# Performance work log

Measured on AMD Instinct MI355X. Metric: run time of the kernel, lower is better.

## Reference

```python
import jax, jax.numpy as jnp
import numpy as np

B, L, S, LA, NA, E, D, H, NHID = 16, 256, 100, 48, 32, 64, 768, 12, 1024
W_IDX = S + 2
EPS = 1e-12


def setup_inputs() -> dict:
    rng = np.random.default_rng(0)
    key = jax.random.key(0)
    ks = jax.random.split(key, 8)
    idxs = np.zeros((B, W_IDX), dtype=np.int64)
    bert_lens = np.zeros((B,), dtype=np.int64)
    is_trig = np.zeros((B, S), dtype=np.float32)
    ent_map = np.zeros((B, S, E), dtype=np.float32)
    argw_mask = np.zeros((B, LA, 1), dtype=np.float32)
    for b in range(B):
        sb = int(rng.integers(60, S + 1))          # n first-subword tokens
        ab = int(rng.integers(8, LA + 1))          # n arg-role subwords
        sent_idx = np.sort(rng.choice(np.arange(1, 2 * sb + 1), size=sb, replace=False))
        sls = 2 * sb + 1                           # second-to-last [SEP] position
        last = sls + ab + 1                        # last [SEP] position
        idxs[b, :sb] = sent_idx
        idxs[b, sb] = sls
        idxs[b, sb + 1] = last
        bert_lens[b] = last + 1
        t0 = int(rng.integers(0, sb - 1))
        is_trig[b, t0:t0 + 2] = 1.0
        eb = int(rng.integers(16, E + 1))
        for e in range(eb):
            ent_map[b, int(rng.integers(0, sb)), e] = 1.0
        argw_mask[b, :ab, 0] = 1.0
    arg_w = np.asarray(jax.random.uniform(ks[0], (B, LA, NA), dtype=jnp.float32)) * argw_mask
    return {
        'all_embeddings': jax.random.normal(ks[1], (B, L, D), dtype=jnp.float32),
        'is_triggers': jnp.asarray(is_trig),
        'arg_weight_matrices': jnp.asarray(arg_w, dtype=jnp.float32),
        'entity_mapping': jnp.asarray(ent_map),
        'att0': jax.random.uniform(ks[2], (B, H, L, L), dtype=jnp.float32),
        'att1': jax.random.uniform(ks[3], (B, H, L, L), dtype=jnp.float32),
        'att2': jax.random.uniform(ks[4], (B, H, L, L), dtype=jnp.float32),
        'W_ta': jax.random.normal(ks[5], (3 * D, D), dtype=jnp.float32) * 0.02,
        'b_ta': jnp.zeros((D,), dtype=jnp.float32),
        'W1': jax.random.normal(ks[6], (6 * D, NHID), dtype=jnp.float32) * 0.02,
        'b1': jnp.zeros((NHID,), dtype=jnp.float32),
        'W2': jax.random.normal(ks[7], (NHID, 1), dtype=jnp.float32) * 0.02,
        'b2': jnp.zeros((1,), dtype=jnp.float32),
        'idxs_to_collect': jnp.asarray(idxs),
        'bert_sentence_lengths': jnp.asarray(bert_lens),
    }


def _l1_normalize(x, axis):
    # F.normalize(x, p=1, dim=axis)
    return x / jnp.clip(jnp.sum(jnp.abs(x), axis=axis, keepdims=True), EPS)


def reference(all_embeddings, is_triggers, arg_weight_matrices, entity_mapping,
              att0, att1, att2, W_ta, b_ta, W1, b1, W2, b2,
              idxs_to_collect, bert_sentence_lengths):
    idxs = idxs_to_collect
    valid = idxs > 0                                   # [B,W]
    n_valid = jnp.sum(valid, axis=1)                   # [B]
    j = jnp.arange(S)
    sent_valid = (j[None, :] < (n_valid - 2)[:, None]).astype(all_embeddings.dtype)  # [B,S]
    sent_idx = idxs[:, :S]
    # first-subword gather, zero-padded (get_fist_subword_embeddings)
    sent_emb = jnp.take_along_axis(all_embeddings, sent_idx[:, :, None], axis=1) * sent_valid[:, :, None]
    # arg-role segment: (second_last_sep+1) .. (bert_len-2), zero-padded to LA
    sls = jnp.take_along_axis(idxs, (n_valid - 2)[:, None], axis=1)[:, 0]   # [B]
    arg_pos = sls[:, None] + 1 + jnp.arange(LA)[None, :]                    # [B,LA]
    arg_valid = (arg_pos < (bert_sentence_lengths - 1)[:, None]).astype(all_embeddings.dtype)
    arg_emb0 = jnp.take_along_axis(all_embeddings, jnp.clip(arg_pos, 0, L - 1)[:, :, None], axis=1) * arg_valid[:, :, None]
    # entity aggregation + trigger mean pooling
    entity = jnp.einsum('bsd,bse->bed', sent_emb, entity_mapping)           # [B,E,D]
    trig = jnp.sum(sent_emb * is_triggers[:, :, None], axis=1) / jnp.sum(is_triggers, axis=1)[:, None]
    arg = jnp.einsum('bld,bla->bad', arg_emb0, arg_weight_matrices)         # [B,NA,D]
    # trigger-aware entity fusion
    trig_e = jnp.broadcast_to(trig[:, None, :], entity.shape)
    nonempty = (jnp.sum(jnp.abs(entity), axis=-1) > 0).astype(entity.dtype)
    ent_cat = jnp.concatenate([entity, trig_e, entity * trig_e], axis=-1)   # [B,E,3D]
    entity = (ent_cat @ W_ta + b_ta) * nonempty[:, :, None]
    # bidirectional token<->arg attention (L1-normalized)
    score = jnp.einsum('bed,bad->bea', entity, arg) / np.sqrt(D)            # [B,E,NA]
    t2a = _l1_normalize(score, 2)[..., None]
    a2t = _l1_normalize(score, 1)[..., None]
    token_argAwared = jnp.sum(arg[:, None] * t2a, axis=2)                   # [B,E,D]
    arg_tokenAwared = jnp.sum(entity[:, :, None] * a2t, axis=1)             # [B,NA,D]
    # select_hidden_att: head-mean, gather collected rows/cols, row-renormalize
    def sel_att(att):
        m = jnp.mean(att, axis=1)                                           # [B,L,L]
        r = jnp.take_along_axis(m, sent_idx[:, :, None], axis=1)            # [B,S,L]
        c = jnp.take_along_axis(r, sent_idx[:, None, :], axis=2)            # [B,S,S]
        c = c * sent_valid[:, :, None] * sent_valid[:, None, :]
        return c / jnp.clip(jnp.sum(c, axis=-1, keepdims=True), EPS)
    t2t = (sel_att(att0) + sel_att(att1) + sel_att(att2)) / 3.0             # [B,S,S]
    a_h2h_tok = t2t @ sent_emb                                              # [B,S,D]
    A_h2h = jnp.einsum('bse,bsd->bed', entity_mapping, a_h2h_tok)           # [B,E,D]
    H_ = jnp.einsum('bse,bsd->bed', entity_mapping, sent_emb)               # [B,E,D]
    a2a = jax.nn.softmax(arg @ jnp.swapaxes(arg, -1, -2), axis=-1)
    A_u2u = a2a @ arg                                                       # [B,NA,D]
    shp = (B, E, NA, D)
    latent = jnp.concatenate([
        jnp.broadcast_to(H_[:, :, None], shp),
        jnp.broadcast_to(arg[:, None], shp),
        jnp.broadcast_to(token_argAwared[:, :, None], shp),
        jnp.broadcast_to(A_h2h[:, :, None], shp),
        jnp.broadcast_to(arg_tokenAwared[:, None], shp),
        jnp.broadcast_to(A_u2u[:, None], shp),
    ], axis=-1)                                                             # [B,E,NA,6D]
    h = jax.nn.gelu(latent @ W1 + b1, approximate=False)
    out = (h @ W2 + b2)[..., 0]                                             # [B,E,NA]
    return out
```

## Files before the change

kernel.cpp:

```cpp
#include <hip/hip_runtime.h>
#include <math.h>

#define B_ 16
#define L_ 256
#define S_ 100
#define LA_ 48
#define NA_ 32
#define E_ 64
#define D_ 768
#define H_ 12
#define NHID_ 1024
#define WIDX_ 102
#define EPSF 1e-12f

typedef __attribute__((ext_vector_type(8))) short s16x8;
typedef __attribute__((ext_vector_type(4))) float f32x4;

__device__ __forceinline__ void split_bf16(float x, unsigned short& h, unsigned short& l) {
  unsigned u = __float_as_uint(x);
  unsigned hr = u + 0x7FFFu + ((u >> 16) & 1u);
  h = (unsigned short)(hr >> 16);
  float r = x - __uint_as_float(hr & 0xFFFF0000u);
  unsigned u2 = __float_as_uint(r);
  unsigned lr = u2 + 0x7FFFu + ((u2 >> 16) & 1u);
  l = (unsigned short)(lr >> 16);
}

__global__ void k_meta(const int* __restrict__ idxs, const int* __restrict__ blen,
                       int* __restrict__ meta) {
  int b = blockIdx.x, t = threadIdx.x;
  __shared__ int cnt;
  if (t == 0) cnt = 0;
  __syncthreads();
  if (t < WIDX_ && idxs[b * WIDX_ + t] > 0) atomicAdd(&cnt, 1);
  __syncthreads();
  if (t == 0) {
    int sb = cnt - 2;
    meta[b * 4 + 0] = sb;
    meta[b * 4 + 1] = idxs[b * WIDX_ + sb];
    meta[b * 4 + 2] = blen[b] - 1;
  }
}

__global__ void k_gather(const float* __restrict__ emb, const int* __restrict__ idxs,
                         const int* __restrict__ meta, float* __restrict__ sent_emb,
                         float* __restrict__ arg_emb) {
  int b = blockIdx.y, y = blockIdx.x, t = threadIdx.x;
  int sb = meta[b * 4 + 0], sls = meta[b * 4 + 1], last = meta[b * 4 + 2];
  if (y < S_) {
    int s = y;
    float* dst = sent_emb + ((size_t)b * S_ + s) * D_;
    if (s < sb) {
      const float* src = emb + ((size_t)b * L_ + idxs[b * WIDX_ + s]) * D_;
      for (int d = t; d < D_; d += 256) dst[d] = src[d];
    } else {
      for (int d = t; d < D_; d += 256) dst[d] = 0.f;
    }
  } else {
    int l = y - S_;
    int pos = sls + 1 + l;
    float* dst = arg_emb + ((size_t)b * LA_ + l) * D_;
    if (pos < last) {
      int p = pos > (L_ - 1) ? (L_ - 1) : pos;
      const float* src = emb + ((size_t)b * L_ + p) * D_;
      for (int d = t; d < D_; d += 256) dst[d] = src[d];
    } else {
      for (int d = t; d < D_; d += 256) dst[d] = 0.f;
    }
  }
}

__global__ void k_trig(const float* __restrict__ sent_emb, const float* __restrict__ is_trig,
                       float* __restrict__ trig) {
  int b = blockIdx.y;
  int d = blockIdx.x * 256 + threadIdx.x;
  float acc = 0.f, den = 0.f;
  for (int s = 0; s < S_; s++) {
    float w = is_trig[b * S_ + s];
    den += w;
    if (w != 0.f) acc += w * sent_emb[((size_t)b * S_ + s) * D_ + d];
  }
  trig[b * D_ + d] = acc / den;
}

__global__ __launch_bounds__(256) void k_entity0(const float* __restrict__ sent_emb,
                                                 const float* __restrict__ ent_map,
                                                 const float* __restrict__ trig,
                                                 unsigned short* __restrict__ e0h,
                                                 unsigned short* __restrict__ e0l,
                                                 unsigned short* __restrict__ e0th,
                                                 unsigned short* __restrict__ e0tl,
                                                 float* __restrict__ ne) {
  int b = blockIdx.y, e = blockIdx.x, t = threadIdx.x;
  float a0 = 0.f, a1 = 0.f, a2 = 0.f;
  for (int s = 0; s < S_; s++) {
    float w = ent_map[((size_t)b * S_ + s) * E_ + e];
    if (w != 0.f) {
      const float* r = sent_emb + ((size_t)b * S_ + s) * D_;
      a0 += w * r[t]; a1 += w * r[t + 256]; a2 += w * r[t + 512];
    }
  }
  size_t o = ((size_t)b * E_ + e) * D_;
  const float* tr = trig + b * D_;
  unsigned short h, lo;
  split_bf16(a0, h, lo); e0h[o + t] = h; e0l[o + t] = lo;
  split_bf16(a1, h, lo); e0h[o + t + 256] = h; e0l[o + t + 256] = lo;
  split_bf16(a2, h, lo); e0h[o + t + 512] = h; e0l[o + t + 512] = lo;
  split_bf16(a0 * tr[t], h, lo); e0th[o + t] = h; e0tl[o + t] = lo;
  split_bf16(a1 * tr[t + 256], h, lo); e0th[o + t + 256] = h; e0tl[o + t + 256] = lo;
  split_bf16(a2 * tr[t + 512], h, lo); e0th[o + t + 512] = h; e0tl[o + t + 512] = lo;
  __shared__ float red[256];
  red[t] = fabsf(a0) + fabsf(a1) + fabsf(a2);
  __syncthreads();
  for (int s2 = 128; s2 > 0; s2 >>= 1) {
    if (t < s2) red[t] += red[t + s2];
    __syncthreads();
  }
  if (t == 0) ne[b * E_ + e] = (red[0] > 0.f) ? 1.f : 0.f;
}

__global__ __launch_bounds__(256) void k_wsum(const float* __restrict__ Wm, int wstride, int sy,
                                              int sx, const float* __restrict__ Vm,
                                              float* __restrict__ Om,
                                              unsigned short* __restrict__ oh,
                                              unsigned short* __restrict__ ol, int Y) {
  int b = blockIdx.y, x = blockIdx.x, t = threadIdx.x;
  float a0 = 0.f, a1 = 0.f, a2 = 0.f;
  const float* wb = Wm + (size_t)b * wstride + (size_t)x * sx;
  const float* vb = Vm + (size_t)b * Y * D_;
  for (int y = 0; y < Y; y++) {
    float w = wb[(size_t)y * sy];
    if (w != 0.f) {
      const float* r = vb + (size_t)y * D_;
      a0 += w * r[t]; a1 += w * r[t + 256]; a2 += w * r[t + 512];
    }
  }
  size_t oidx = ((size_t)b * gridDim.x + x) * D_;
  if (Om) {
    Om[oidx + t] = a0; Om[oidx + t + 256] = a1; Om[oidx + t + 512] = a2;
  }
  if (oh) {
    unsigned short h, lo;
    split_bf16(a0, h, lo); oh[oidx + t] = h; ol[oidx + t] = lo;
    split_bf16(a1, h, lo); oh[oidx + t + 256] = h; ol[oidx + t + 256] = lo;
    split_bf16(a2, h, lo); oh[oidx + t + 512] = h; ol[oidx + t + 512] = lo;
  }
}

__global__ void k_tb(const float* __restrict__ trig, const float* __restrict__ W_ta,
                     const float* __restrict__ b_ta, float* __restrict__ tb) {
  int b = blockIdx.y;
  int d = blockIdx.x * 256 + threadIdx.x;
  float acc0 = b_ta[d], acc1 = 0.f, acc2 = 0.f, acc3 = 0.f;
  float acc4 = 0.f, acc5 = 0.f, acc6 = 0.f, acc7 = 0.f;
  const float* tr = trig + b * D_;
  const float* w = W_ta + (size_t)D_ * D_ + d;
  for (int k = 0; k < D_; k += 8) {
    acc0 += tr[k + 0] * w[(size_t)(k + 0) * D_];
    acc1 += tr[k + 1] * w[(size_t)(k + 1) * D_];
    acc2 += tr[k + 2] * w[(size_t)(k + 2) * D_];
    acc3 += tr[k + 3] * w[(size_t)(k + 3) * D_];
    acc4 += tr[k + 4] * w[(size_t)(k + 4) * D_];
    acc5 += tr[k + 5] * w[(size_t)(k + 5) * D_];
    acc6 += tr[k + 6] * w[(size_t)(k + 6) * D_];
    acc7 += tr[k + 7] * w[(size_t)(k + 7) * D_];
  }
  tb[b * D_ + d] = ((acc0 + acc1) + (acc2 + acc3)) + ((acc4 + acc5) + (acc6 + acc7));
}

__global__ __launch_bounds__(256) void k_cvtT(const float* __restrict__ src, int K, int N,
                                              unsigned short* __restrict__ th,
                                              unsigned short* __restrict__ tl) {
  __shared__ float tile[32][33];
  int k0 = blockIdx.x * 32, n0 = blockIdx.y * 32;
  int tr = threadIdx.x >> 3, c4 = (threadIdx.x & 7) * 4;
  float4 v = *(const float4*)(src + (size_t)(k0 + tr) * N + n0 + c4);
  tile[tr][c4] = v.x; tile[tr][c4 + 1] = v.y; tile[tr][c4 + 2] = v.z; tile[tr][c4 + 3] = v.w;
  __syncthreads();
  unsigned short h[4], l[4];
#pragma unroll
  for (int i = 0; i < 4; ++i) split_bf16(tile[c4 + i][tr], h[i], l[i]);
  size_t oo = (size_t)(n0 + tr) * K + k0 + c4;
  th[oo + 0] = h[0]; th[oo + 1] = h[1]; th[oo + 2] = h[2]; th[oo + 3] = h[3];
  tl[oo + 0] = l[0]; tl[oo + 1] = l[1]; tl[oo + 2] = l[2]; tl[oo + 3] = l[3];
}

__global__ __launch_bounds__(256) void k_mgemm(
    int phase,
    const unsigned short* __restrict__ e0h, const unsigned short* __restrict__ e0l,
    const unsigned short* __restrict__ e0th, const unsigned short* __restrict__ e0tl,
    const unsigned short* __restrict__ Ah2hh, const unsigned short* __restrict__ Ah2hl,
    const unsigned short* __restrict__ argmh, const unsigned short* __restrict__ argml,
    const unsigned short* __restrict__ Au2uh, const unsigned short* __restrict__ Au2ul,
    const unsigned short* __restrict__ WtaTh, const unsigned short* __restrict__ WtaTl,
    const unsigned short* __restrict__ W1Th, const unsigned short* __restrict__ W1Tl,
    float* __restrict__ entn, unsigned short* __restrict__ entnh,
    unsigned short* __restrict__ entnl,
    float* __restrict__ PeA, float* __restrict__ PaA,
    float* __restrict__ P2, float* __restrict__ Q2,
    const float* __restrict__ tb, const float* __restrict__ ne) {
  int z = blockIdx.z;
  const unsigned short *A0h_, *A0l_, *A1h_, *A1l_, *Bh_, *Bl_;
  float* C;
  int koff0, koff1, bstride, mtiles, niter, N, ep = 0;
  if (phase == 0) {
    if (z == 0) {
      A0h_ = e0h; A0l_ = e0l; A1h_ = e0th; A1l_ = e0tl; Bh_ = WtaTh; Bl_ = WtaTl;
      bstride = 2304; koff0 = 0; koff1 = 1536; C = entn; N = 768; mtiles = 16; niter = 48; ep = 1;
    } else if (z == 1) {
      A0h_ = e0h; A0l_ = e0l; A1h_ = Ah2hh; A1l_ = Ah2hl; Bh_ = W1Th; Bl_ = W1Tl;
      bstride = 4608; koff0 = 0; koff1 = 3 * 768; C = PeA; N = 1024; mtiles = 16; niter = 48;
    } else if (z == 2) {
      A0h_ = argmh; A0l_ = argml; A1h_ = Au2uh; A1l_ = Au2ul; Bh_ = W1Th; Bl_ = W1Tl;
      bstride = 4608; koff0 = 768; koff1 = 5 * 768; C = PaA; N = 1024; mtiles = 8; niter = 48;
    } else {
      A0h_ = argmh; A0l_ = argml; A1h_ = argmh; A1l_ = argml; Bh_ = W1Th; Bl_ = W1Tl;
      bstride = 4608; koff0 = 2 * 768; koff1 = 2 * 768; C = P2; N = 1024; mtiles = 8; niter = 24;
    }
  } else {
    A0h_ = entnh; A0l_ = entnl; A1h_ = entnh; A1l_ = entnl; Bh_ = W1Th; Bl_ = W1Tl;
    bstride = 4608; koff0 = 4 * 768; koff1 = 4 * 768; C = Q2; N = 1024; mtiles = 16; niter = 24;
  }
  int bx = blockIdx.x, by = blockIdx.y;
  if (by >= mtiles || bx * 64 >= N) return;

  __shared__ unsigned short As[2][64][4][8];
  __shared__ unsigned short Bs[2][64][4][8];

  int tid = threadIdx.x;
  int srow = tid >> 2, sg = tid & 3;
  int wc = sg ^ ((srow >> 1) & 3);
  size_t aoff = (size_t)(by * 64 + srow) * 768 + sg * 8;
  size_t brow = (size_t)(bx * 64 + srow) * bstride + sg * 8;
  size_t boff0 = brow + koff0, boff1 = brow + koff1;

  s16x8 rAh = *(const s16x8*)(A0h_ + aoff);
  s16x8 rAl = *(const s16x8*)(A0l_ + aoff);
  s16x8 rBh = *(const s16x8*)(Bh_ + boff0);
  s16x8 rBl = *(const s16x8*)(Bl_ + boff0);

  int lane = tid & 63, wave = tid >> 6;
  int wm = wave >> 1, wn = wave & 1;
  int fg = lane >> 4, fr = lane & 15;
  int ar0 = wm * 32 + fr;
  int bc0 = wn * 32 + fr;
  int ca = fg ^ ((ar0 >> 1) & 3);
  int cb = fg ^ ((bc0 >> 1) & 3);

  f32x4 acc00 = {0.f, 0.f, 0.f, 0.f}, acc01 = {0.f, 0.f, 0.f, 0.f};
  f32x4 acc10 = {0.f, 0.f, 0.f, 0.f}, acc11 = {0.f, 0.f, 0.f, 0.f};

  for (int it = 0; it < niter; ++it) {
    __syncthreads();
    *(s16x8*)&As[0][srow][wc][0] = rAh;
    *(s16x8*)&As[1][srow][wc][0] = rAl;
    *(s16x8*)&Bs[0][srow][wc][0] = rBh;
    *(s16x8*)&Bs[1][srow][wc][0] = rBl;
    __syncthreads();
    if (it + 1 < niter) {
      int l = it + 1;
      int p = (l >= 24) ? 1 : 0;
      size_t ka = (size_t)(l - (p ? 24 : 0)) * 32;
      rAh = *(const s16x8*)((p ? A1h_ : A0h_) + aoff + ka);
      rAl = *(const s16x8*)((p ? A1l_ : A0l_) + aoff + ka);
      size_t bo = (p ? boff1 : boff0) + ka;
      rBh = *(const s16x8*)(Bh_ + bo);
      rBl = *(const s16x8*)(Bl_ + bo);
    }
    s16x8 ah0 = *(const s16x8*)&As[0][ar0][ca][0];
    s16x8 ah1 = *(const s16x8*)&As[0][ar0 + 16][ca][0];
    s16x8 al0 = *(const s16x8*)&As[1][ar0][ca][0];
    s16x8 al1 = *(const s16x8*)&As[1][ar0 + 16][ca][0];
    s16x8 bh0 = *(const s16x8*)&Bs[0][bc0][cb][0];
    s16x8 bh1 = *(const s16x8*)&Bs[0][bc0 + 16][cb][0];
    s16x8 bl0 = *(const s16x8*)&Bs[1][bc0][cb][0];
    s16x8 bl1 = *(const s16x8*)&Bs[1][bc0 + 16][cb][0];
    acc00 = __builtin_amdgcn_mfma_f32_16x16x32_bf16(ah0, bh0, acc00, 0, 0, 0);
    acc00 = __builtin_amdgcn_mfma_f32_16x16x32_bf16(ah0, bl0, acc00, 0, 0, 0);
    acc00 = __builtin_amdgcn_mfma_f32_16x16x32_bf16(al0, bh0, acc00, 0, 0, 0);
    acc01 = __builtin_amdgcn_mfma_f32_16x16x32_bf16(ah0, bh1, acc01, 0, 0, 0);
    acc01 = __builtin_amdgcn_mfma_f32_16x16x32_bf16(ah0, bl1, acc01, 0, 0, 0);
    acc01 = __builtin_amdgcn_mfma_f32_16x16x32_bf16(al0, bh1, acc01, 0, 0, 0);
    acc10 = __builtin_amdgcn_mfma_f32_16x16x32_bf16(ah1, bh0, acc10, 0, 0, 0);
    acc10 = __builtin_amdgcn_mfma_f32_16x16x32_bf16(ah1, bl0, acc10, 0, 0, 0);
    acc10 = __builtin_amdgcn_mfma_f32_16x16x32_bf16(al1, bh0, acc10, 0, 0, 0);
    acc11 = __builtin_amdgcn_mfma_f32_16x16x32_bf16(ah1, bh1, acc11, 0, 0, 0);
    acc11 = __builtin_amdgcn_mfma_f32_16x16x32_bf16(ah1, bl1, acc11, 0, 0, 0);
    acc11 = __builtin_amdgcn_mfma_f32_16x16x32_bf16(al1, bh1, acc11, 0, 0, 0);
  }

  f32x4 accs[2][2] = {{acc00, acc01}, {acc10, acc11}};
  int colb = bx * 64 + wn * 32 + fr;
  int rowb = by * 64 + wm * 32 + fg * 4;
#pragma unroll
  for (int i = 0; i < 2; ++i) {
#pragma unroll
    for (int j = 0; j < 2; ++j) {
      int col = colb + j * 16;
#pragma unroll
      for (int r = 0; r < 4; ++r) {
        int row = rowb + i * 16 + r;
        float v = accs[i][j][r];
        if (ep == 1) {
          v = (v + tb[(row >> 6) * D_ + col]) * ne[row];
          unsigned short hh, ll;
          split_bf16(v, hh, ll);
          entnh[(size_t)row * D_ + col] = hh;
          entnl[(size_t)row * D_ + col] = ll;
        }
        C[(size_t)row * N + col] = v;
      }
    }
  }
}

__global__ __launch_bounds__(256) void k_score(const float* __restrict__ entn,
                                               const float* __restrict__ argm,
                                               float* __restrict__ score) {
  int b = blockIdx.y, e = blockIdx.x, t = threadIdx.x;
  __shared__ float ent[D_];
  const float* er = entn + ((size_t)b * E_ + e) * D_;
  for (int d = t; d < D_; d += 256) ent[d] = er[d];
  __syncthreads();
  int wave = t >> 6, lane = t & 63;
  const float scale = 0.03608439182435161f;
  for (int a = wave; a < NA_; a += 4) {
    const float* ar = argm + ((size_t)b * NA_ + a) * D_;
    float p = 0.f;
#pragma unroll
    for (int i = 0; i < 12; i++) {
      int d = lane + 64 * i;
      p += ent[d] * ar[d];
    }
    for (int off = 32; off > 0; off >>= 1) p += __shfl_down(p, off);
    if (lane == 0) score[((size_t)b * E_ + e) * NA_ + a] = p * scale;
  }
}

__global__ void k_norm(const float* __restrict__ score, float* __restrict__ t2a,
                       float* __restrict__ a2t) {
  int b = blockIdx.x, t = threadIdx.x;
  __shared__ float s[E_ * NA_];
  __shared__ float rs[E_];
  __shared__ float cs[NA_];
  for (int i = t; i < E_ * NA_; i += 256) s[i] = score[(size_t)b * E_ * NA_ + i];
  __syncthreads();
  if (t < E_) {
    float sum = 0.f;
    for (int a = 0; a < NA_; a++) sum += fabsf(s[t * NA_ + a]);
    rs[t] = fmaxf(sum, EPSF);
  } else if (t >= 64 && t < 96) {
    int a = t - 64;
    float sum = 0.f;
    for (int e = 0; e < E_; e++) sum += fabsf(s[e * NA_ + a]);
    cs[a] = fmaxf(sum, EPSF);
  }
  __syncthreads();
  for (int i = t; i < E_ * NA_; i += 256) {
    int e = i >> 5, a = i & 31;
    float v = s[i];
    t2a[(size_t)b * E_ * NA_ + i] = v / rs[e];
    a2t[(size_t)b * E_ * NA_ + i] = v / cs[a];
  }
}

__global__ __launch_bounds__(256) void k_a2a(const float* __restrict__ argm,
                                             float* __restrict__ a2a) {
  int b = blockIdx.y, a = blockIdx.x, t = threadIdx.x;
  __shared__ float sA[D_];
  __shared__ float lg[NA_];
  const float* ar = argm + ((size_t)b * NA_ + a) * D_;
  for (int d = t; d < D_; d += 256) sA[d] = ar[d];
  __syncthreads();
  int wave = t >> 6, lane = t & 63;
  for (int a2 = wave; a2 < NA_; a2 += 4) {
    const float* br = argm + ((size_t)b * NA_ + a2) * D_;
    float p = 0.f;
#pragma unroll
    for (int i = 0; i < 12; i++) {
      int d = lane + 64 * i;
      p += sA[d] * br[d];
    }
    for (int off = 32; off > 0; off >>= 1) p += __shfl_down(p, off);
    if (lane == 0) lg[a2] = p;
  }
  __syncthreads();
  if (t < 64) {
    float v = (t < NA_) ? lg[t] : -INFINITY;
    float m = v;
    for (int mask = 16; mask > 0; mask >>= 1) m = fmaxf(m, __shfl_xor(m, mask));
    float ex = (t < NA_) ? expf(v - m) : 0.f;
    float sm = ex;
    for (int mask = 16; mask > 0; mask >>= 1) sm += __shfl_xor(sm, mask);
    if (t < NA_) a2a[((size_t)b * NA_ + a) * NA_ + t] = ex / sm;
  }
}

__global__ __launch_bounds__(128) void k_t2t(const float* __restrict__ att0,
                                             const float* __restrict__ att1,
                                             const float* __restrict__ att2,
                                             const int* __restrict__ idxs,
                                             const int* __restrict__ meta,
                                             float* __restrict__ t2t) {
  int b = blockIdx.y, s = blockIdx.x, t = threadIdx.x;
  int sb = meta[b * 4 + 0];
  float* out = t2t + ((size_t)b * S_ + s) * S_;
  if (s >= sb) {
    for (int j = t; j < S_; j += 128) out[j] = 0.f;
    return;
  }
  int Is = idxs[b * WIDX_ + s];
  int It = (t < S_) ? idxs[b * WIDX_ + t] : 0;
  __shared__ float row[256];
  __shared__ float red[128];
  const float* atts[3] = {att0, att1, att2};
  float accout = 0.f;
  for (int q = 0; q < 3; q++) {
    float r0 = 0.f, r1 = 0.f;
    const float* base = atts[q] + (((size_t)b * H_) * L_ + Is) * L_;
    for (int h = 0; h < H_; h++) {
      const float* rp = base + (size_t)h * L_ * L_;
      r0 += rp[t];
      r1 += rp[t + 128];
    }
    row[t] = r0;
    row[t + 128] = r1;
    __syncthreads();
    float v = (t < sb) ? row[It] * (1.f / 12.f) : 0.f;
    red[t] = v;
    __syncthreads();
    for (int s2 = 64; s2 > 0; s2 >>= 1) {
      if (t < s2) red[t] += red[t + s2];
      __syncthreads();
    }
    float rsum = red[0];
    __syncthreads();
    accout += v / fmaxf(rsum, EPSF) * (1.f / 3.f);
  }
  if (t < S_) out[t] = accout;
}

__global__ __launch_bounds__(256) void k_mix(const float* __restrict__ PeA,
                                             const float* __restrict__ PaA,
                                             const float* __restrict__ P2,
                                             const float* __restrict__ Q2,
                                             const float* __restrict__ t2a,
                                             const float* __restrict__ a2t,
                                             const float* __restrict__ b1,
                                             float* __restrict__ ps, float* __restrict__ qs) {
  int b = blockIdx.y, x = blockIdx.x, t = threadIdx.x;
  int n0 = t * 4;
  __shared__ float w[E_];
  if (x < E_) {
    int e = x;
    size_t ro = ((size_t)b * E_ + e) * NHID_ + n0;
    float4 acc = *(const float4*)(PeA + ro);
    float4 bb = *(const float4*)(b1 + n0);
    acc.x += bb.x; acc.y += bb.y; acc.z += bb.z; acc.w += bb.w;
    if (t < NA_) w[t] = t2a[((size_t)b * E_ + e) * NA_ + t];
    __syncthreads();
    const float* pb = P2 + (size_t)b * NA_ * NHID_ + n0;
#pragma unroll 4
    for (int a = 0; a < NA_; a++) {
      float ww = w[a];
      float4 p = *(const float4*)(pb + (size_t)a * NHID_);
      acc.x += ww * p.x; acc.y += ww * p.y; acc.z += ww * p.z; acc.w += ww * p.w;
    }
    *(float4*)(ps + ro) = acc;
  } else {
    int a = x - E_;
    size_t ro = ((size_t)b * NA_ + a) * NHID_ + n0;
    float4 acc = *(const float4*)(PaA + ro);
    for (int i = t; i < E_; i += 256) w[i] = a2t[((size_t)b * E_ + i) * NA_ + a];
    __syncthreads();
    const float* qb = Q2 + (size_t)b * E_ * NHID_ + n0;
#pragma unroll 4
    for (int e = 0; e < E_; e++) {
      float ww = w[e];
      float4 q = *(const float4*)(qb + (size_t)e * NHID_);
      acc.x += ww * q.x; acc.y += ww * q.y; acc.z += ww * q.z; acc.w += ww * q.w;
    }
    *(float4*)(qs + ro) = acc;
  }
}

__global__ __launch_bounds__(256) void k_final(const float* __restrict__ ps,
                                               const float* __restrict__ qs,
                                               const float* __restrict__ W2,
                                               const float* __restrict__ b2,
                                               float* __restrict__ out) {
  int b = blockIdx.y, e = blockIdx.x, t = threadIdx.x;
  int wave = t >> 6, lane = t & 63;
  const float ks = 0.70710678118654752f;
  size_t po = ((size_t)b * E_ + e) * NHID_ + lane * 4;
  float4 p0 = *(const float4*)(ps + po);
  float4 p1 = *(const float4*)(ps + po + 256);
  float4 p2 = *(const float4*)(ps + po + 512);
  float4 p3 = *(const float4*)(ps + po + 768);
  const float* w2p = W2 + lane * 4;
  float4 w0 = *(const float4*)(w2p);
  float4 w1 = *(const float4*)(w2p + 256);
  float4 w2 = *(const float4*)(w2p + 512);
  float4 w3 = *(const float4*)(w2p + 768);
  __shared__ float outs[NA_];
#pragma unroll 2
  for (int a = wave; a < NA_; a += 4) {
    size_t qo = ((size_t)b * NA_ + a) * NHID_ + lane * 4;
    float4 q0 = *(const float4*)(qs + qo);
    float4 q1 = *(const float4*)(qs + qo + 256);
    float4 q2 = *(const float4*)(qs + qo + 512);
    float4 q3 = *(const float4*)(qs + qo + 768);
    float acc = 0.f;
#define GEL4(pp, qq, ww)                                          \
    {                                                             \
      float x0 = pp.x + qq.x, x1 = pp.y + qq.y;                   \
      float x2 = pp.z + qq.z, x3 = pp.w + qq.w;                   \
      float g0 = 0.5f * x0 * (1.f + erff(x0 * ks));               \
      float g1 = 0.5f * x1 * (1.f + erff(x1 * ks));               \
      float g2 = 0.5f * x2 * (1.f + erff(x2 * ks));               \
      float g3 = 0.5f * x3 * (1.f + erff(x3 * ks));               \
      acc += g0 * ww.x + g1 * ww.y + g2 * ww.z + g3 * ww.w;       \
    }
    GEL4(p0, q0, w0)
    GEL4(p1, q1, w1)
    GEL4(p2, q2, w2)
    GEL4(p3, q3, w3)
#undef GEL4
    acc += __shfl_xor(acc, 32);
    acc += __shfl_xor(acc, 16);
    acc += __shfl_xor(acc, 8);
    acc += __shfl_xor(acc, 4);
    acc += __shfl_xor(acc, 2);
    acc += __shfl_xor(acc, 1);
    if (lane == 0) outs[a] = acc;
  }
  __syncthreads();
  if (t < NA_) out[((size_t)b * E_ + e) * NA_ + t] = outs[t] + b2[0];
}

extern "C" void kernel_launch(void* const* d_in, const int* in_sizes, int n_in,
                              void* d_out, int out_size, void* d_ws, size_t ws_size,
                              hipStream_t stream) {
  const float* emb    = (const float*)d_in[0];
  const float* istrig = (const float*)d_in[1];
  const float* argw   = (const float*)d_in[2];
  const float* entmap = (const float*)d_in[3];
  const float* att0   = (const float*)d_in[4];
  const float* att1   = (const float*)d_in[5];
  const float* att2   = (const float*)d_in[6];
  const float* W_ta   = (const float*)d_in[7];
  const float* b_ta   = (const float*)d_in[8];
  const float* W1     = (const float*)d_in[9];
  const float* b1     = (const float*)d_in[10];
  const float* W2     = (const float*)d_in[11];
  const float* b2     = (const float*)d_in[12];
  const int*   idxs   = (const int*)d_in[13];
  const int*   blen   = (const int*)d_in[14];
  float* out = (float*)d_out;

  float* ws = (float*)d_ws;
  size_t o = 0;
  int* meta = (int*)ws; o += 256;
  float* sent_emb = ws + o; o += (size_t)B_ * S_ * D_;
  float* arg_emb  = ws + o; o += (size_t)B_ * LA_ * D_;
  float* trig     = ws + o; o += (size_t)B_ * D_;
  float* argm     = ws + o; o += (size_t)B_ * NA_ * D_;
  float* entn     = ws + o; o += (size_t)B_ * E_ * D_;
  float* tb       = ws + o; o += (size_t)B_ * D_;
  float* ne       = ws + o; o += (size_t)B_ * E_;
  float* score    = ws + o; o += (size_t)B_ * E_ * NA_;
  float* t2a      = ws + o; o += (size_t)B_ * E_ * NA_;
  float* a2t      = ws + o; o += (size_t)B_ * E_ * NA_;
  float* t2t      = ws + o; o += (size_t)B_ * S_ * S_;
  float* ah2h     = ws + o; o += (size_t)B_ * S_ * D_;
  float* a2a      = ws + o; o += (size_t)B_ * NA_ * NA_;
  float* PeA      = ws + o; o += (size_t)B_ * E_ * NHID_;
  float* PaA      = ws + o; o += (size_t)B_ * NA_ * NHID_;
  float* P2       = ws + o; o += (size_t)B_ * NA_ * NHID_;
  float* Q2       = ws + o; o += (size_t)B_ * E_ * NHID_;
  float* ps = sent_emb;
  float* qs = arg_emb;

  o = (o + 3) & ~(size_t)3;
  unsigned short* us = (unsigned short*)(ws + o);
  size_t uo = 0;
  unsigned short* e0h   = us + uo; uo += (size_t)B_ * E_ * D_;
  unsigned short* e0l   = us + uo; uo += (size_t)B_ * E_ * D_;
  unsigned short* e0th  = us + uo; uo += (size_t)B_ * E_ * D_;
  unsigned short* e0tl  = us + uo; uo += (size_t)B_ * E_ * D_;
  unsigned short* Ah2hh = us + uo; uo += (size_t)B_ * E_ * D_;
  unsigned short* Ah2hl = us + uo; uo += (size_t)B_ * E_ * D_;
  unsigned short* argmh = us + uo; uo += (size_t)B_ * NA_ * D_;
  unsigned short* argml = us + uo; uo += (size_t)B_ * NA_ * D_;
  unsigned short* Au2uh = us + uo; uo += (size_t)B_ * NA_ * D_;
  unsigned short* Au2ul = us + uo; uo += (size_t)B_ * NA_ * D_;
  unsigned short* entnh = us + uo; uo += (size_t)B_ * E_ * D_;
  unsigned short* entnl = us + uo; uo += (size_t)B_ * E_ * D_;
  unsigned short* WtaTh = us + uo; uo += (size_t)2304 * 768;
  unsigned short* WtaTl = us + uo; uo += (size_t)2304 * 768;
  unsigned short* W1Th  = us + uo; uo += (size_t)4608 * 1024;
  unsigned short* W1Tl  = us + uo; uo += (size_t)4608 * 1024;

  k_meta<<<B_, 128, 0, stream>>>(idxs, blen, meta);
  k_cvtT<<<dim3(2304 / 32, 768 / 32), 256, 0, stream>>>(W_ta, 2304, 768, WtaTh, WtaTl);
  k_cvtT<<<dim3(4608 / 32, 1024 / 32), 256, 0, stream>>>(W1, 4608, 1024, W1Th, W1Tl);
  k_gather<<<dim3(S_ + LA_, B_), 256, 0, stream>>>(emb, idxs, meta, sent_emb, arg_emb);
  k_trig<<<dim3(3, B_), 256, 0, stream>>>(sent_emb, istrig, trig);
  k_entity0<<<dim3(E_, B_), 256, 0, stream>>>(sent_emb, entmap, trig, e0h, e0l, e0th, e0tl, ne);
  k_wsum<<<dim3(NA_, B_), 256, 0, stream>>>(argw, LA_ * NA_, NA_, 1, arg_emb, argm, argmh,
                                            argml, LA_);
  k_tb<<<dim3(3, B_), 256, 0, stream>>>(trig, W_ta, b_ta, tb);
  k_t2t<<<dim3(S_, B_), 128, 0, stream>>>(att0, att1, att2, idxs, meta, t2t);
  k_wsum<<<dim3(S_, B_), 256, 0, stream>>>(t2t, S_ * S_, 1, S_, sent_emb, ah2h, nullptr,
                                           nullptr, S_);
  k_wsum<<<dim3(E_, B_), 256, 0, stream>>>(entmap, S_ * E_, E_, 1, ah2h, nullptr, Ah2hh,
                                           Ah2hl, S_);
  k_a2a<<<dim3(NA_, B_), 256, 0, stream>>>(argm, a2a);
  k_wsum<<<dim3(NA_, B_), 256, 0, stream>>>(a2a, NA_ * NA_, 1, NA_, argm, nullptr, Au2uh,
                                            Au2ul, NA_);

  k_mgemm<<<dim3(16, 16, 4), 256, 0, stream>>>(0, e0h, e0l, e0th, e0tl, Ah2hh, Ah2hl, argmh,
                                               argml, Au2uh, Au2ul, WtaTh, WtaTl, W1Th, W1Tl,
                                               entn, entnh, entnl, PeA, PaA, P2, Q2, tb, ne);

  k_mgemm<<<dim3(16, 16, 1), 256, 0, stream>>>(1, e0h, e0l, e0th, e0tl, Ah2hh, Ah2hl, argmh,
                                               argml, Au2uh, Au2ul, WtaTh, WtaTl, W1Th, W1Tl,
                                               entn, entnh, entnl, PeA, PaA, P2, Q2, tb, ne);

  k_score<<<dim3(E_, B_), 256, 0, stream>>>(entn, argm, score);
  k_norm<<<B_, 256, 0, stream>>>(score, t2a, a2t);
  k_mix<<<dim3(E_ + NA_, B_), 256, 0, stream>>>(PeA, PaA, P2, Q2, t2a, a2t, b1, ps, qs);

  k_final<<<dim3(E_, B_), 256, 0, stream>>>(ps, qs, W2, b2, out);
}
```

Before: 504.9 us.

## Split-K the batched MFMA GEMMs and double-buffer LDS tiles

Each GEMM job in k_mgemm is split into two K halves run as separate z-slices, which doubles the number of blocks. Each half writes a partial result to its own buffer. The partials are summed later, in a new k_combE kernel for the entity projection and inside k_mix for the W1 partials. The main loop now uses double-buffered LDS with register prefetch two tiles ahead, so it needs one barrier per tile instead of two. The aim is better occupancy on the small 64x64-tile grids and shorter per-block latency, at the cost of extra partial-buffer traffic and one more launch.

```diff
diff --git a/kernel.cpp b/kernel.cpp
--- a/kernel.cpp
+++ b/kernel.cpp
@@ -192,52 +192,55 @@
     const unsigned short* __restrict__ Ah2hh, const unsigned short* __restrict__ Ah2hl,
     const unsigned short* __restrict__ argmh, const unsigned short* __restrict__ argml,
     const unsigned short* __restrict__ Au2uh, const unsigned short* __restrict__ Au2ul,
+    const unsigned short* __restrict__ entnh, const unsigned short* __restrict__ entnl,
     const unsigned short* __restrict__ WtaTh, const unsigned short* __restrict__ WtaTl,
     const unsigned short* __restrict__ W1Th, const unsigned short* __restrict__ W1Tl,
-    float* __restrict__ entn, unsigned short* __restrict__ entnh,
-    unsigned short* __restrict__ entnl,
-    float* __restrict__ PeA, float* __restrict__ PaA,
-    float* __restrict__ P2, float* __restrict__ Q2,
-    const float* __restrict__ tb, const float* __restrict__ ne) {
+    float* __restrict__ Cpe, float* __restrict__ PeAp, float* __restrict__ PaAp,
+    float* __restrict__ P2p, float* __restrict__ Q2p) {
   int z = blockIdx.z;
-  const unsigned short *A0h_, *A0l_, *A1h_, *A1l_, *Bh_, *Bl_;
+  const unsigned short *Ah_, *Al_, *Bh_, *Bl_;
   float* C;
-  int koff0, koff1, bstride, mtiles, niter, N, ep = 0;
+  int bstride, mtiles, niter, N, akoff, bkoff;
+  const size_t HPE = (size_t)B_ * E_ * NHID_;
+  const size_t HPA = (size_t)B_ * NA_ * NHID_;
   if (phase == 0) {
-    if (z == 0) {
-      A0h_ = e0h; A0l_ = e0l; A1h_ = e0th; A1l_ = e0tl; Bh_ = WtaTh; Bl_ = WtaTl;
-      bstride = 2304; koff0 = 0; koff1 = 1536; C = entn; N = 768; mtiles = 16; niter = 48; ep = 1;
-    } else if (z == 1) {
-      A0h_ = e0h; A0l_ = e0l; A1h_ = Ah2hh; A1l_ = Ah2hl; Bh_ = W1Th; Bl_ = W1Tl;
-      bstride = 4608; koff0 = 0; koff1 = 3 * 768; C = PeA; N = 1024; mtiles = 16; niter = 48;
-    } else if (z == 2) {
-      A0h_ = argmh; A0l_ = argml; A1h_ = Au2uh; A1l_ = Au2ul; Bh_ = W1Th; Bl_ = W1Tl;
-      bstride = 4608; koff0 = 768; koff1 = 5 * 768; C = PaA; N = 1024; mtiles = 8; niter = 48;
+    int job = z >> 1, kh = z & 1;
+    if (job == 0) {
+      Ah_ = kh ? e0th : e0h; Al_ = kh ? e0tl : e0l; Bh_ = WtaTh; Bl_ = WtaTl;
+      bstride = 2304; akoff = 0; bkoff = kh ? 1536 : 0;
+      C = Cpe + (size_t)kh * 1024 * 768; N = 768; mtiles = 16; niter = 24;
+    } else if (job == 1) {
+      Ah_ = kh ? Ah2hh : e0h; Al_ = kh ? Ah2hl : e0l; Bh_ = W1Th; Bl_ = W1Tl;
+      bstride = 4608; akoff = 0; bkoff = kh ? 3 * 768 : 0;
+      C = PeAp + kh * HPE; N = 1024; mtiles = 16; niter = 24;
+    } else if (job == 2) {
+      Ah_ = kh ? Au2uh : argmh; Al_ = kh ? Au2ul : argml; Bh_ = W1Th; Bl_ = W1Tl;
+      bstride = 4608; akoff = 0; bkoff = kh ? 5 * 768 : 768;
+      C = PaAp + kh * HPA; N = 1024; mtiles = 8; niter = 24;
     } else {
-      A0h_ = argmh; A0l_ = argml; A1h_ = argmh; A1l_ = argml; Bh_ = W1Th; Bl_ = W1Tl;
-      bstride = 4608; koff0 = 2 * 768; koff1 = 2 * 768; C = P2; N = 1024; mtiles = 8; niter = 24;
+      Ah_ = argmh; Al_ = argml; Bh_ = W1Th; Bl_ = W1Tl;
+      bstride = 4608; akoff = kh * 384; bkoff = 2 * 768 + kh * 384;
+      C = P2p + kh * HPA; N = 1024; mtiles = 8; niter = 12;
     }
   } else {
-    A0h_ = entnh; A0l_ = entnl; A1h_ = entnh; A1l_ = entnl; Bh_ = W1Th; Bl_ = W1Tl;
-    bstride = 4608; koff0 = 4 * 768; koff1 = 4 * 768; C = Q2; N = 1024; mtiles = 16; niter = 24;
+    int kh = z;
+    Ah_ = entnh; Al_ = entnl; Bh_ = W1Th; Bl_ = W1Tl;
+    bstride = 4608; akoff = kh * 384; bkoff = 4 * 768 + kh * 384;
+    C = Q2p + kh * HPE; N = 1024; mtiles = 16; niter = 12;
   }
   int bx = blockIdx.x, by = blockIdx.y;
   if (by >= mtiles || bx * 64 >= N) return;
 
-  __shared__ unsigned short As[2][64][4][8];
-  __shared__ unsigned short Bs[2][64][4][8];
+  __shared__ unsigned short As[2][2][64][4][8];
+  __shared__ unsigned short Bs[2][2][64][4][8];
 
   int tid = threadIdx.x;
   int srow = tid >> 2, sg = tid & 3;
   int wc = sg ^ ((srow >> 1) & 3);
-  size_t aoff = (size_t)(by * 64 + srow) * 768 + sg * 8;
-  size_t brow = (size_t)(bx * 64 + srow) * bstride + sg * 8;
-  size_t boff0 = brow + koff0, boff1 = brow + koff1;
-
-  s16x8 rAh = *(const s16x8*)(A0h_ + aoff);
-  s16x8 rAl = *(const s16x8*)(A0l_ + aoff);
-  s16x8 rBh = *(const s16x8*)(Bh_ + boff0);
-  s16x8 rBl = *(const s16x8*)(Bl_ + boff0);
+  const unsigned short* aPh = Ah_ + (size_t)(by * 64 + srow) * 768 + akoff + sg * 8;
+  const unsigned short* aPl = Al_ + (size_t)(by * 64 + srow) * 768 + akoff + sg * 8;
+  const unsigned short* bPh = Bh_ + (size_t)(bx * 64 + srow) * bstride + bkoff + sg * 8;
+  const unsigned short* bPl = Bl_ + (size_t)(bx * 64 + srow) * bstride + bkoff + sg * 8;
 
   int lane = tid & 63, wave = tid >> 6;
   int wm = wave >> 1, wn = wave & 1;
@@ -250,44 +253,70 @@
   f32x4 acc00 = {0.f, 0.f, 0.f, 0.f}, acc01 = {0.f, 0.f, 0.f, 0.f};
   f32x4 acc10 = {0.f, 0.f, 0.f, 0.f}, acc11 = {0.f, 0.f, 0.f, 0.f};
 
-  for (int it = 0; it < niter; ++it) {
-    __syncthreads();
-    *(s16x8*)&As[0][srow][wc][0] = rAh;
-    *(s16x8*)&As[1][srow][wc][0] = rAl;
-    *(s16x8*)&Bs[0][srow][wc][0] = rBh;
-    *(s16x8*)&Bs[1][srow][wc][0] = rBl;
-    __syncthreads();
+  s16x8 a0h = *(const s16x8*)(aPh + 0), a0l = *(const s16x8*)(aPl + 0);
+  s16x8 b0h = *(const s16x8*)(bPh + 0), b0l = *(const s16x8*)(bPl + 0);
+  s16x8 a1h = *(const s16x8*)(aPh + 32), a1l = *(const s16x8*)(aPl + 32);
+  s16x8 b1h = *(const s16x8*)(bPh + 32), b1l = *(const s16x8*)(bPl + 32);
+
+#define WRITE_LDS(buf, ah, al, bh, bl)              \
+  {                                                 \
+    *(s16x8*)&As[buf][0][srow][wc][0] = ah;         \
+    *(s16x8*)&As[buf][1][srow][wc][0] = al;         \
+    *(s16x8*)&Bs[buf][0][srow][wc][0] = bh;         \
+    *(s16x8*)&Bs[buf][1][srow][wc][0] = bl;         \
+  }
+#define LOAD_SET(ah, al, bh, bl, t_)                \
+  {                                                 \
+    ah = *(const s16x8*)(aPh + (t_) * 32);          \
+    al = *(const s16x8*)(aPl + (t_) * 32);          \
+    bh = *(const s16x8*)(bPh + (t_) * 32);          \
+    bl = *(const s16x8*)(bPl + (t_) * 32);          \
+  }
+#define READ_MFMA(buf)                                                          \
+  {                                                                             \
+    s16x8 xah0 = *(const s16x8*)&As[buf][0][ar0][ca][0];                        \
+    s16x8 xah1 = *(const s16x8*)&As[buf][0][ar0 + 16][ca][0];                   \
+    s16x8 xal0 = *(const s16x8*)&As[buf][1][ar0][ca][0];                        \
+    s16x8 xal1 = *(const s16x8*)&As[buf][1][ar0 + 16][ca][0];                   \
+    s16x8 xbh0 = *(const s16x8*)&Bs[buf][0][bc0][cb][0];                        \
+    s16x8 xbh1 = *(const s16x8*)&Bs[buf][0][bc0 + 16][cb][0];                   \
+    s16x8 xbl0 = *(const s16x8*)&Bs[buf][1][bc0][cb][0];                        \
+    s16x8 xbl1 = *(const s16x8*)&Bs[buf][1][bc0 + 16][cb][0];                   \
+    acc00 = __builtin_amdgcn_mfma_f32_16x16x32_bf16(xah0, xbh0, acc00, 0, 0, 0); \
+    acc00 = __builtin_amdgcn_mfma_f32_16x16x32_bf16(xah0, xbl0, acc00, 0, 0, 0); \
+    acc00 = __builtin_amdgcn_mfma_f32_16x16x32_bf16(xal0, xbh0, acc00, 0, 0, 0); \
+    acc01 = __builtin_amdgcn_mfma_f32_16x16x32_bf16(xah0, xbh1, acc01, 0, 0, 0); \
+    acc01 = __builtin_amdgcn_mfma_f32_16x16x32_bf16(xah0, xbl1, acc01, 0, 0, 0); \
+    acc01 = __builtin_amdgcn_mfma_f32_16x16x32_bf16(xal0, xbh1, acc01, 0, 0, 0); \
+    acc10 = __builtin_amdgcn_mfma_f32_16x16x32_bf16(xah1, xbh0, acc10, 0, 0, 0); \
+    acc10 = __builtin_amdgcn_mfma_f32_16x16x32_bf16(xah1, xbl0, acc10, 0, 0, 0); \
+    acc10 = __builtin_amdgcn_mfma_f32_16x16x32_bf16(xal1, xbh0, acc10, 0, 0, 0); \
+    acc11 = __builtin_amdgcn_mfma_f32_16x16x32_bf16(xah1, xbh1, acc11, 0, 0, 0); \
+    acc11 = __builtin_amdgcn_mfma_f32_16x16x32_bf16(xah1, xbl1, acc11, 0, 0, 0); \
+    acc11 = __builtin_amdgcn_mfma_f32_16x16x32_bf16(xal1, xbh1, acc11, 0, 0, 0); \
+  }
+
+  WRITE_LDS(0, a0h, a0l, b0h, b0l);
+  LOAD_SET(a0h, a0l, b0h, b0l, 2);
+  __syncthreads();
+
+  for (int it = 0; it < niter; it += 2) {
     if (it + 1 < niter) {
-      int l = it + 1;
-      int p = (l >= 24) ? 1 : 0;
-      size_t ka = (size_t)(l - (p ? 24 : 0)) * 32;
-      rAh = *(const s16x8*)((p ? A1h_ : A0h_) + aoff + ka);
-      rAl = *(const s16x8*)((p ? A1l_ : A0l_) + aoff + ka);
-      size_t bo = (p ? boff1 : boff0) + ka;
-      rBh = *(const s16x8*)(Bh_ + bo);
-      rBl = *(const s16x8*)(Bl_ + bo);
-    }
-    s16x8 ah0 = *(const s16x8*)&As[0][ar0][ca][0];
-    s16x8 ah1 = *(const s16x8*)&As[0][ar0 + 16][ca][0];
-    s16x8 al0 = *(const s16x8*)&As[1][ar0][ca][0];
-    s16x8 al1 = *(const s16x8*)&As[1][ar0 + 16][ca][0];
-    s16x8 bh0 = *(const s16x8*)&Bs[0][bc0][cb][0];
-    s16x8 bh1 = *(const s16x8*)&Bs[0][bc0 + 16][cb][0];
-    s16x8 bl0 = *(const s16x8*)&Bs[1][bc0][cb][0];
-    s16x8 bl1 = *(const s16x8*)&Bs[1][bc0 + 16][cb][0];
-    acc00 = __builtin_amdgcn_mfma_f32_16x16x32_bf16(ah0, bh0, acc00, 0, 0, 0);
-    acc00 = __builtin_amdgcn_mfma_f32_16x16x32_bf16(ah0, bl0, acc00, 0, 0, 0);
-    acc00 = __builtin_amdgcn_mfma_f32_16x16x32_bf16(al0, bh0, acc00, 0, 0, 0);
-    acc01 = __builtin_amdgcn_mfma_f32_16x16x32_bf16(ah0, bh1, acc01, 0, 0, 0);
-    acc01 = __builtin_amdgcn_mfma_f32_16x16x32_bf16(ah0, bl1, acc01, 0, 0, 0);
-    acc01 = __builtin_amdgcn_mfma_f32_16x16x32_bf16(al0, bh1, acc01, 0, 0, 0);
-    acc10 = __builtin_amdgcn_mfma_f32_16x16x32_bf16(ah1, bh0, acc10, 0, 0, 0);
-    acc10 = __builtin_amdgcn_mfma_f32_16x16x32_bf16(ah1, bl0, acc10, 0, 0, 0);
-    acc10 = __builtin_amdgcn_mfma_f32_16x16x32_bf16(al1, bh0, acc10, 0, 0, 0);
-    acc11 = __builtin_amdgcn_mfma_f32_16x16x32_bf16(ah1, bh1, acc11, 0, 0, 0);
-    acc11 = __builtin_amdgcn_mfma_f32_16x16x32_bf16(ah1, bl1, acc11, 0, 0, 0);
-    acc11 = __builtin_amdgcn_mfma_f32_16x16x32_bf16(al1, bh1, acc11, 0, 0, 0);
-  }
+      WRITE_LDS(1, a1h, a1l, b1h, b1l);
+      if (it + 3 < niter) LOAD_SET(a1h, a1l, b1h, b1l, it + 3);
+    }
+    READ_MFMA(0);
+    __syncthreads();
+    if (it + 2 < niter) {
+      WRITE_LDS(0, a0h, a0l, b0h, b0l);
+      if (it + 4 < niter) LOAD_SET(a0h, a0l, b0h, b0l, it + 4);
+    }
+    READ_MFMA(1);
+    __syncthreads();
+  }
+#undef WRITE_LDS
+#undef LOAD_SET
+#undef READ_MFMA
 
   f32x4 accs[2][2] = {{acc00, acc01}, {acc10, acc11}};
   int colb = bx * 64 + wn * 32 + fr;
@@ -300,16 +329,35 @@
 #pragma unroll
       for (int r = 0; r < 4; ++r) {
         int row = rowb + i * 16 + r;
-        float v = accs[i][j][r];
-        if (ep == 1) {
-          v = (v + tb[(row >> 6) * D_ + col]) * ne[row];
-          unsigned short hh, ll;
-          split_bf16(v, hh, ll);
-          entnh[(size_t)row * D_ + col] = hh;
-          entnl[(size_t)row * D_ + col] = ll;
-        }
-        C[(size_t)row * N + col] = v;
+        C[(size_t)row * N + col] = accs[i][j][r];
       }
+    }
+  }
+}
+
+__global__ __launch_bounds__(256) void k_combE(const float* __restrict__ Cpe,
+                                               const float* __restrict__ tb,
+                                               const float* __restrict__ ne,
+                                               float* __restrict__ entn,
+                                               unsigned short* __restrict__ entnh,
+                                               unsigned short* __restrict__ entnl) {
+  int t = threadIdx.x;
+  int r0 = blockIdx.x * 4;
+  const size_t HH = (size_t)1024 * 768;
+#pragma unroll
+  for (int i = 0; i < 4; ++i) {
+    int row = r0 + i;
+    int b = row >> 6;
+    float nev = ne[row];
+#pragma unroll
+    for (int j = 0; j < 3; ++j) {
+      int col = t + j * 256;
+      size_t o = (size_t)row * D_ + col;
+      float v = (Cpe[o] + Cpe[HH + o] + tb[(size_t)b * D_ + col]) * nev;
+      entn[o] = v;
+      unsigned short hh, ll;
+      split_bf16(v, hh, ll);
+      entnh[o] = hh; entnl[o] = ll;
     }
   }
 }
@@ -440,45 +488,55 @@
   if (t < S_) out[t] = accout;
 }
 
-__global__ __launch_bounds__(256) void k_mix(const float* __restrict__ PeA,
-                                             const float* __restrict__ PaA,
-                                             const float* __restrict__ P2,
-                                             const float* __restrict__ Q2,
+__global__ __launch_bounds__(256) void k_mix(const float* __restrict__ PeAp,
+                                             const float* __restrict__ PaAp,
+                                             const float* __restrict__ P2p,
+                                             const float* __restrict__ Q2p,
                                              const float* __restrict__ t2a,
                                              const float* __restrict__ a2t,
                                              const float* __restrict__ b1,
                                              float* __restrict__ ps, float* __restrict__ qs) {
   int b = blockIdx.y, x = blockIdx.x, t = threadIdx.x;
   int n0 = t * 4;
+  const size_t HPE = (size_t)B_ * E_ * NHID_;
+  const size_t HPA = (size_t)B_ * NA_ * NHID_;
   __shared__ float w[E_];
   if (x < E_) {
     int e = x;
     size_t ro = ((size_t)b * E_ + e) * NHID_ + n0;
-    float4 acc = *(const float4*)(PeA + ro);
+    float4 acc = *(const float4*)(PeAp + ro);
+    float4 u1 = *(const float4*)(PeAp + HPE + ro);
     float4 bb = *(const float4*)(b1 + n0);
-    acc.x += bb.x; acc.y += bb.y; acc.z += bb.z; acc.w += bb.w;
+    acc.x += u1.x + bb.x; acc.y += u1.y + bb.y;
+    acc.z += u1.z + bb.z; acc.w += u1.w + bb.w;
     if (t < NA_) w[t] = t2a[((size_t)b * E_ + e) * NA_ + t];
     __syncthreads();
-    const float* pb = P2 + (size_t)b * NA_ * NHID_ + n0;
-#pragma unroll 4
+    const float* pb = P2p + (size_t)b * NA_ * NHID_ + n0;
+#pragma unroll 2
     for (int a = 0; a < NA_; a++) {
       float ww = w[a];
-      float4 p = *(const float4*)(pb + (size_t)a * NHID_);
-      acc.x += ww * p.x; acc.y += ww * p.y; acc.z += ww * p.z; acc.w += ww * p.w;
+      float4 p0v = *(const float4*)(pb + (size_t)a * NHID_);
+      float4 p1v = *(const float4*)(pb + HPA + (size_t)a * NHID_);
+      acc.x += ww * (p0v.x + p1v.x); acc.y += ww * (p0v.y + p1v.y);
+      acc.z += ww * (p0v.z + p1v.z); acc.w += ww * (p0v.w + p1v.w);
     }
     *(float4*)(ps + ro) = acc;
   } else {
     int a = x - E_;
     size_t ro = ((size_t)b * NA_ + a) * NHID_ + n0;
-    float4 acc = *(const float4*)(PaA + ro);
+    float4 acc = *(const float4*)(PaAp + ro);
+    float4 u1 = *(const float4*)(PaAp + HPA + ro);
+    acc.x += u1.x; acc.y += u1.y; acc.z += u1.z; acc.w += u1.w;
     for (int i = t; i < E_; i += 256) w[i] = a2t[((size_t)b * E_ + i) * NA_ + a];
     __syncthreads();
-    const float* qb = Q2 + (size_t)b * E_ * NHID_ + n0;
-#pragma unroll 4
+    const float* qb = Q2p + (size_t)b * E_ * NHID_ + n0;
+#pragma unroll 2
     for (int e = 0; e < E_; e++) {
       float ww = w[e];
-      float4 q = *(const float4*)(qb + (size_t)e * NHID_);
-      acc.x += ww * q.x; acc.y += ww * q.y; acc.z += ww * q.z; acc.w += ww * q.w;
+      float4 q0v = *(const float4*)(qb + (size_t)e * NHID_);
+      float4 q1v = *(const float4*)(qb + HPE + (size_t)e * NHID_);
+      acc.x += ww * (q0v.x + q1v.x); acc.y += ww * (q0v.y + q1v.y);
+      acc.z += ww * (q0v.z + q1v.z); acc.w += ww * (q0v.w + q1v.w);
     }
     *(float4*)(qs + ro) = acc;
   }
@@ -574,10 +632,11 @@
   float* t2t      = ws + o; o += (size_t)B_ * S_ * S_;
   float* ah2h     = ws + o; o += (size_t)B_ * S_ * D_;
   float* a2a      = ws + o; o += (size_t)B_ * NA_ * NA_;
-  float* PeA      = ws + o; o += (size_t)B_ * E_ * NHID_;
-  float* PaA      = ws + o; o += (size_t)B_ * NA_ * NHID_;
-  float* P2       = ws + o; o += (size_t)B_ * NA_ * NHID_;
-  float* Q2       = ws + o; o += (size_t)B_ * E_ * NHID_;
+  float* Cpe      = ws + o; o += (size_t)2 * 1024 * 768;
+  float* PeAp     = ws + o; o += (size_t)2 * B_ * E_ * NHID_;
+  float* PaAp     = ws + o; o += (size_t)2 * B_ * NA_ * NHID_;
+  float* P2p      = ws + o; o += (size_t)2 * B_ * NA_ * NHID_;
+  float* Q2p      = ws + o; o += (size_t)2 * B_ * E_ * NHID_;
   float* ps = sent_emb;
   float* qs = arg_emb;
 
@@ -619,17 +678,19 @@
   k_wsum<<<dim3(NA_, B_), 256, 0, stream>>>(a2a, NA_ * NA_, 1, NA_, argm, nullptr, Au2uh,
                                             Au2ul, NA_);
 
-  k_mgemm<<<dim3(16, 16, 4), 256, 0, stream>>>(0, e0h, e0l, e0th, e0tl, Ah2hh, Ah2hl, argmh,
-                                               argml, Au2uh, Au2ul, WtaTh, WtaTl, W1Th, W1Tl,
-                                               entn, entnh, entnl, PeA, PaA, P2, Q2, tb, ne);
-
-  k_mgemm<<<dim3(16, 16, 1), 256, 0, stream>>>(1, e0h, e0l, e0th, e0tl, Ah2hh, Ah2hl, argmh,
-                                               argml, Au2uh, Au2ul, WtaTh, WtaTl, W1Th, W1Tl,
-                                               entn, entnh, entnl, PeA, PaA, P2, Q2, tb, ne);
+  k_mgemm<<<dim3(16, 16, 8), 256, 0, stream>>>(0, e0h, e0l, e0th, e0tl, Ah2hh, Ah2hl, argmh,
+                                               argml, Au2uh, Au2ul, entnh, entnl, WtaTh,
+                                               WtaTl, W1Th, W1Tl, Cpe, PeAp, PaAp, P2p, Q2p);
+
+  k_combE<<<dim3(B_ * E_ / 4), 256, 0, stream>>>(Cpe, tb, ne, entn, entnh, entnl);
+
+  k_mgemm<<<dim3(16, 16, 2), 256, 0, stream>>>(1, e0h, e0l, e0th, e0tl, Ah2hh, Ah2hl, argmh,
+                                               argml, Au2uh, Au2ul, entnh, entnl, WtaTh,
+                                               WtaTl, W1Th, W1Tl, Cpe, PeAp, PaAp, P2p, Q2p);
 
   k_score<<<dim3(E_, B_), 256, 0, stream>>>(entn, argm, score);
   k_norm<<<B_, 256, 0, stream>>>(score, t2a, a2t);
-  k_mix<<<dim3(E_ + NA_, B_), 256, 0, stream>>>(PeA, PaA, P2, Q2, t2a, a2t, b1, ps, qs);
+  k_mix<<<dim3(E_ + NA_, B_), 256, 0, stream>>>(PeAp, PaAp, P2p, Q2p, t2a, a2t, b1, ps, qs);
 
   k_final<<<dim3(E_, B_), 256, 0, stream>>>(ps, qs, W2, b2, out);
 }
```

Measured after the change: 510.9 us. About the same (+1.2%).
